# Optimization experiments

Hardware: AMD Instinct MI355X
Metric: run time of the kernel (lower is better)

## Reference

```python
import jax, jax.numpy as jnp
import numpy as np

N = 3072          # number of nodes
IN_DIM = 512
H = 8             # num_heads
D = 64            # out_dim per head
A = 8             # num_angles
CLAMP = 5.0


def setup_inputs() -> dict:
    key = jax.random.key(0)
    ks = jax.random.split(key, 9)
    HD = H * D
    return {
        "x": jax.random.normal(ks[0], (N, IN_DIM), jnp.float32),
        "node_rotation_angles": jax.random.normal(ks[1], (N, A), jnp.float32),
        "Wq": jax.random.normal(ks[2], (IN_DIM, HD), jnp.float32) * 0.05,
        "bq": jnp.zeros((HD,), jnp.float32),
        "Wk": jax.random.normal(ks[3], (IN_DIM, HD), jnp.float32) * 0.05,
        "bk": jnp.zeros((HD,), jnp.float32),
        "Wv": jax.random.normal(ks[4], (IN_DIM, HD), jnp.float32) * 0.05,
        "bv": jnp.zeros((HD,), jnp.float32),
        "S": jax.random.normal(ks[5], (A, HD // 2), jnp.float32),
    }


def reference(x, node_rotation_angles, Wq, bq, Wk, bk, Wv, bv, S):
    n = x.shape[0]
    # QKV projections -> [N, H, D]
    Qh = (x @ Wq + bq).reshape(n, H, D)
    Kh = (x @ Wk + bk).reshape(n, H, D)
    Vh = (x @ Wv + bv).reshape(n, H, D)

    # learned per-node rotation angles: [N, A] @ softmax(S, axis=1) -> [N, H*D/2]
    theta = node_rotation_angles @ jax.nn.softmax(S, axis=1)
    theta = jnp.repeat(theta, 2, axis=1).reshape(n, H, D)
    cos_pos = jnp.cos(theta)
    sin_pos = jnp.sin(theta)

    # torch.stack([-q_odd, q_even], dim=2).reshape -> concat of halves (faithful)
    q2 = jnp.concatenate([-Qh[..., 1::2], Qh[..., ::2]], axis=-1)
    k2 = jnp.concatenate([-Kh[..., 1::2], Kh[..., ::2]], axis=-1)
    Q = Qh * cos_pos + q2 * sin_pos
    K = Kh * cos_pos + k2 * sin_pos

    # faithful to original: raw .view() (reshape), NOT a transpose
    src = K.reshape(H, D, n)    # [H, D, N]
    dest = Q.reshape(H, n, D)   # [H, N, D]

    score = jnp.einsum("hnd,hdm->hnm", dest, src) / (D ** 0.5)
    score = jnp.clip(score, -CLAMP, CLAMP)
    attn = jax.nn.softmax(score, axis=-1)  # [H, N, N]

    # V uses a true transpose in the original
    msg = jnp.einsum("hnm,hmd->hnd", attn, jnp.swapaxes(Vh, 0, 1))
    return jnp.swapaxes(msg, 0, 1)  # [N, H, D]
```

## Files before the change

### kernel.cpp

```cpp
#include <hip/hip_runtime.h>

#define NN     3072
#define IND    512
#define NH     8
#define DH     64
#define HDTOT  512
#define NA     8
#define THALF  256
#define DN     196608

typedef float f32x4 __attribute__((ext_vector_type(4)));
typedef short bf16x8 __attribute__((ext_vector_type(8)));
typedef unsigned int u32x2 __attribute__((ext_vector_type(2)));

__device__ __forceinline__ unsigned short f2bf(float f) {
    union { float f; unsigned u; } a; a.f = f;
    unsigned u = a.u;
    return (unsigned short)((u + 0x7FFFu + ((u >> 16) & 1u)) >> 16);
}
__device__ __forceinline__ unsigned pack2(float a, float b) {
    union { float f; unsigned u; } ua, ub; ua.f = a; ub.f = b;
    unsigned ra = ua.u + 0x7FFFu + ((ua.u >> 16) & 1u);
    unsigned rb = ub.u + 0x7FFFu + ((ub.u >> 16) & 1u);
    return __builtin_amdgcn_perm(rb, ra, 0x07060302);
}
__device__ __forceinline__ float ubits2f(unsigned u) {
    union { unsigned u; float f; } c; c.u = u; return c.f;
}

__global__ __launch_bounds__(256) void k_prep(
    const float* __restrict__ S, const float* __restrict__ x,
    const float* __restrict__ Wq, const float* __restrict__ Wk,
    const float* __restrict__ Wv,
    float* __restrict__ SM, unsigned short* __restrict__ xb,
    unsigned short* __restrict__ WTb)
{
    __shared__ float sh[32 * 33];
    const int b = blockIdx.x, t = threadIdx.x;
    if (b == 0) {
        for (int a = 0; a < NA; ++a) {
            float v = S[a * THALF + t];
            sh[t] = v; __syncthreads();
            for (int s = 128; s > 0; s >>= 1) {
                if (t < s) sh[t] = fmaxf(sh[t], sh[t + s]);
                __syncthreads();
            }
            float mx = sh[0]; __syncthreads();
            float e = __expf(v - mx);
            sh[t] = e; __syncthreads();
            for (int s = 128; s > 0; s >>= 1) {
                if (t < s) sh[t] += sh[t + s];
                __syncthreads();
            }
            float inv = 1.0f / sh[0]; __syncthreads();
            SM[a * THALF + t] = e * inv;
        }
    } else if (b <= 768) {
        const size_t base = ((size_t)(b - 1) * 256 + t) * 8;
        float4 v0 = *reinterpret_cast<const float4*>(&x[base]);
        float4 v1 = *reinterpret_cast<const float4*>(&x[base + 4]);
        uint4 w;
        w.x = pack2(v0.x, v0.y); w.y = pack2(v0.z, v0.w);
        w.z = pack2(v1.x, v1.y); w.w = pack2(v1.z, v1.w);
        *reinterpret_cast<uint4*>(&xb[base]) = w;
    } else {
        const int b2 = b - 769;
        const int kt = b2 & 15, nt = b2 >> 4;
        const int k0 = kt * 32, n0 = nt * 32;
        const float* __restrict__ W = (n0 < 512) ? Wq : (n0 < 1024 ? Wk : Wv);
        const int nc0 = n0 & 511;
        const int r = t >> 5, c = t & 31;
        #pragma unroll
        for (int i = 0; i < 4; ++i)
            sh[(r + i * 8) * 33 + c] = W[(size_t)(k0 + r + i * 8) * HDTOT + nc0 + c];
        __syncthreads();
        #pragma unroll
        for (int i = 0; i < 4; ++i) {
            const int nr = r + i * 8;
            WTb[(size_t)(n0 + nr) * IND + k0 + c] = f2bf(sh[c * 33 + nr]);
        }
    }
}

__global__ __launch_bounds__(256) void k_qkv_mfma(
    const unsigned short* __restrict__ xb,
    const unsigned short* __restrict__ WTb,
    const float* __restrict__ bq, const float* __restrict__ bk,
    const float* __restrict__ bv,
    const float* __restrict__ angles, const float* __restrict__ SM,
    unsigned short* __restrict__ Qb, unsigned short* __restrict__ KTb,
    unsigned short* __restrict__ VTb)
{
    __shared__ __align__(16) char lds[41472];
    char* At  = lds;
    char* Bt  = lds + 16384;
    float* Cs = (float*)lds;
    float* SMl = (float*)(lds + 33280);

    const int t = threadIdx.x;
    const int lane = t & 63;
    const int wv = t >> 6;
    const int wrow = wv >> 1, wcol = wv & 1;
    const int l15 = lane & 15, lg = lane >> 4;
    const int r8 = lane >> 3, c8 = lane & 7;

    const int m0 = blockIdx.x * 128;
    const int n0 = blockIdx.y * 64;
    const int mat = n0 >> 9;
    const int c0 = n0 & 511;

    if (mat < 2) {
        #pragma unroll
        for (int r = 0; r < 8; ++r) SMl[r * 256 + t] = SM[r * 256 + t];
    }

    f32x4 acc[4][2];
    #pragma unroll
    for (int mf = 0; mf < 4; ++mf)
        #pragma unroll
        for (int nf = 0; nf < 2; ++nf)
            acc[mf][nf] = (f32x4){0.f, 0.f, 0.f, 0.f};

    for (int kt = 0; kt < 8; ++kt) {
        __syncthreads();
        #pragma unroll
        for (int i = 0; i < 4; ++i) {
            const int row = wv * 32 + i * 8 + r8;
            const unsigned short* src =
                xb + (size_t)(m0 + row) * IND + kt * 64 + (c8 ^ (row & 7)) * 8;
            __builtin_amdgcn_global_load_lds(
                (const __attribute__((address_space(1))) unsigned int*)src,
                (__attribute__((address_space(3))) unsigned int*)(At + (wv * 32 + i * 8) * 128),
                16, 0, 0);
        }
        #pragma unroll
        for (int i = 0; i < 2; ++i) {
            const int row = wv * 16 + i * 8 + r8;
            const unsigned short* src =
                WTb + (size_t)(n0 + row) * IND + kt * 64 + (c8 ^ (row & 7)) * 8;
            __builtin_amdgcn_global_load_lds(
                (const __attribute__((address_space(1))) unsigned int*)src,
                (__attribute__((address_space(3))) unsigned int*)(Bt + (wv * 16 + i * 8) * 128),
                16, 0, 0);
        }
        __syncthreads();
        #pragma unroll
        for (int ks = 0; ks < 2; ++ks) {
            bf16x8 af[4], bfr[2];
            #pragma unroll
            for (int mf = 0; mf < 4; ++mf) {
                const int row = wrow * 64 + mf * 16 + l15;
                int off = row * 128 + ks * 64 + lg * 16;
                off ^= (row & 7) << 4;
                af[mf] = *reinterpret_cast<const bf16x8*>(At + off);
            }
            #pragma unroll
            for (int nf = 0; nf < 2; ++nf) {
                const int row = wcol * 32 + nf * 16 + l15;
                int off = row * 128 + ks * 64 + lg * 16;
                off ^= (row & 7) << 4;
                bfr[nf] = *reinterpret_cast<const bf16x8*>(Bt + off);
            }
            #pragma unroll
            for (int mf = 0; mf < 4; ++mf)
                #pragma unroll
                for (int nf = 0; nf < 2; ++nf)
                    acc[mf][nf] = __builtin_amdgcn_mfma_f32_16x16x32_bf16(
                        af[mf], bfr[nf], acc[mf][nf], 0, 0, 0);
        }
    }

    if (mat == 2) {
        #pragma unroll
        for (int nf = 0; nf < 2; ++nf) {
            const int cg = c0 + wcol * 32 + nf * 16 + l15;
            const float b = bv[cg];
            const int hV = cg >> 6, dd = cg & 63;
            #pragma unroll
            for (int mf = 0; mf < 4; ++mf) {
                const int nb = m0 + wrow * 64 + mf * 16 + lg * 4;
                u32x2 w;
                w.x = pack2(acc[mf][nf][0] + b, acc[mf][nf][1] + b);
                w.y = pack2(acc[mf][nf][2] + b, acc[mf][nf][3] + b);
                *reinterpret_cast<u32x2*>(&VTb[(size_t)hV * DN + (size_t)dd * NN + nb]) = w;
            }
        }
        return;
    }

    __syncthreads();
    const float* __restrict__ bsv = mat ? bk : bq;
    #pragma unroll
    for (int nf = 0; nf < 2; ++nf) {
        const int colc = wcol * 32 + nf * 16 + l15;
        const float b = bsv[c0 + colc];
        #pragma unroll
        for (int mf = 0; mf < 4; ++mf) {
            const int rb = wrow * 64 + mf * 16 + lg * 4;
            #pragma unroll
            for (int r = 0; r < 4; ++r)
                Cs[(rb + r) * 65 + colc] = acc[mf][nf][r] + b;
        }
    }
    __syncthreads();

    const int ni0 = (t & 15) * 4;
    const int rbase = (t >> 4) * 8;
    const int pidx = (c0 + ni0) >> 1;
    const int hK = m0 / 384;
    const float QS = 0.1803368801111204f;

    #pragma unroll
    for (int rr = 0; rr < 8; ++rr) {
        const int row = rbase + rr;
        const int n = m0 + row;
        const float4 a0 = *reinterpret_cast<const float4*>(&angles[n * NA]);
        const float4 a1 = *reinterpret_cast<const float4*>(&angles[n * NA + 4]);
        float th0, th1;
        th0 = a0.x * SMl[0 * 256 + pidx];
        th0 = fmaf(a0.y, SMl[1 * 256 + pidx], th0);
        th0 = fmaf(a0.z, SMl[2 * 256 + pidx], th0);
        th0 = fmaf(a0.w, SMl[3 * 256 + pidx], th0);
        th0 = fmaf(a1.x, SMl[4 * 256 + pidx], th0);
        th0 = fmaf(a1.y, SMl[5 * 256 + pidx], th0);
        th0 = fmaf(a1.z, SMl[6 * 256 + pidx], th0);
        th0 = fmaf(a1.w, SMl[7 * 256 + pidx], th0);
        th1 = a0.x * SMl[0 * 256 + pidx + 1];
        th1 = fmaf(a0.y, SMl[1 * 256 + pidx + 1], th1);
        th1 = fmaf(a0.z, SMl[2 * 256 + pidx + 1], th1);
        th1 = fmaf(a0.w, SMl[3 * 256 + pidx + 1], th1);
        th1 = fmaf(a1.x, SMl[4 * 256 + pidx + 1], th1);
        th1 = fmaf(a1.y, SMl[5 * 256 + pidx + 1], th1);
        th1 = fmaf(a1.z, SMl[6 * 256 + pidx + 1], th1);
        th1 = fmaf(a1.w, SMl[7 * 256 + pidx + 1], th1);
        float s0, c0f, s1, c1f;
        __sincosf(th0, &s0, &c0f);
        __sincosf(th1, &s1, &c1f);
        float o[4];
        #pragma unroll
        for (int cc = 0; cc < 4; ++cc) {
            const int d = ni0 + cc;
            const int pd = (d < 32) ? (2 * d + 1) : (2 * (d - 32));
            float own = Cs[row * 65 + d];
            float pv  = Cs[row * 65 + pd];
            float q2  = (d < 32) ? -pv : pv;
            float ct  = (cc < 2) ? c0f : c1f;
            float st  = (cc < 2) ? s0 : s1;
            o[cc] = own * ct + q2 * st;
        }
        if (mat == 0) {
            u32x2 w;
            w.x = pack2(o[0] * QS, o[1] * QS);
            w.y = pack2(o[2] * QS, o[3] * QS);
            *reinterpret_cast<u32x2*>(&Qb[(size_t)n * HDTOT + c0 + ni0]) = w;
        } else {
            const int nn = n - hK * 384;
            const int dk = nn / 6;
            const int jb = (nn - dk * 6) * 512 + c0 + ni0;
            #pragma unroll
            for (int cc = 0; cc < 4; ++cc)
                KTb[(size_t)hK * DN + (size_t)(jb + cc) * 64 + dk] = f2bf(o[cc]);
        }
    }
}

template<int TILES, bool PARTIAL>
__global__ __launch_bounds__(128) void k_attn(
    const unsigned short* __restrict__ Qb,
    const unsigned short* __restrict__ KTb,
    const unsigned short* __restrict__ VTb,
    float* __restrict__ outp, float* __restrict__ Dp)
{
    __shared__ __align__(16) char smem[24576];
    const int t = threadIdx.x;
    const int lane = t & 63;
    const int wv = t >> 6;
    char* ktl = smem;
    char* vtl = smem + 8192;
    char* ptw = smem + 16384 + wv * 4096;

    const int h = blockIdx.y;
    const int qbase = blockIdx.x * 64;
    const int z = blockIdx.z;
    const int jt0 = z * TILES;
    const int l15 = lane & 15;
    const int lg = lane >> 4;
    const int r8 = lane >> 3;
    const int c8 = lane & 7;

    const float CLP = 7.2134752044448170f;

    const int X  = (l15 & 7) << 4;
    const int A0 = l15 * 128 + ((lg * 16) ^ X);
    const int A1 = l15 * 128 + ((64 + lg * 16) ^ X);
    const int W0 = l15 * 128 + ((lg * 8) ^ X);
    const int W1 = l15 * 128 + ((32 + lg * 8) ^ X);
    const int W2 = l15 * 128 + ((64 + lg * 8) ^ X);
    const int W3 = l15 * 128 + ((96 + lg * 8) ^ X);

    bf16x8 qf[2][2];
    #pragma unroll
    for (int im = 0; im < 2; ++im)
        #pragma unroll
        for (int ks = 0; ks < 2; ++ks) {
            const int i = qbase + wv * 32 + im * 16 + l15;
            qf[im][ks] = *reinterpret_cast<const bf16x8*>(
                Qb + (size_t)h * DN + (size_t)i * 64 + ks * 32 + lg * 8);
        }

    f32x4 oacc[2][4];
    #pragma unroll
    for (int im = 0; im < 2; ++im)
        #pragma unroll
        for (int db = 0; db < 4; ++db)
            oacc[im][db] = (f32x4){0.f, 0.f, 0.f, 0.f};
    float dpart[2] = {0.f, 0.f};

    for (int jj = 0; jj < TILES; ++jj) {
        const int j0 = (jt0 + jj) * 64;
        #pragma unroll
        for (int cc = 0; cc < 4; ++cc) {
            const int row = wv * 32 + cc * 8 + r8;
            const int chunk = c8 ^ (row & 7);
            const unsigned short* srcK =
                KTb + (size_t)h * DN + (size_t)(j0 + row) * 64 + chunk * 8;
            __builtin_amdgcn_global_load_lds(
                (const __attribute__((address_space(1))) unsigned int*)srcK,
                (__attribute__((address_space(3))) unsigned int*)(ktl + (wv * 32 + cc * 8) * 128),
                16, 0, 0);
            const unsigned short* srcV =
                VTb + (size_t)h * DN + (size_t)row * NN + j0 + chunk * 8;
            __builtin_amdgcn_global_load_lds(
                (const __attribute__((address_space(1))) unsigned int*)srcV,
                (__attribute__((address_space(3))) unsigned int*)(vtl + (wv * 32 + cc * 8) * 128),
                16, 0, 0);
        }
        __syncthreads();

        f32x4 sac[2][4];
        #pragma unroll
        for (int im = 0; im < 2; ++im)
            #pragma unroll
            for (int jb = 0; jb < 4; ++jb)
                sac[im][jb] = (f32x4){0.f, 0.f, 0.f, 0.f};
        #pragma unroll
        for (int ks = 0; ks < 2; ++ks) {
            const int Aks = ks ? A1 : A0;
            bf16x8 kf[4];
            #pragma unroll
            for (int jb = 0; jb < 4; ++jb)
                kf[jb] = *reinterpret_cast<const bf16x8*>(ktl + Aks + jb * 2048);
            #pragma unroll
            for (int im = 0; im < 2; ++im)
                #pragma unroll
                for (int jb = 0; jb < 4; ++jb)
                    sac[im][jb] = __builtin_amdgcn_mfma_f32_16x16x32_bf16(
                        kf[jb], qf[im][ks], sac[im][jb], 0, 0, 0);
        }

        #pragma unroll
        for (int im = 0; im < 2; ++im) {
            #pragma unroll
            for (int jb = 0; jb < 4; ++jb) {
                float p[4];
                #pragma unroll
                for (int r = 0; r < 4; ++r) {
                    float sc = __builtin_amdgcn_fmed3f(sac[im][jb][r], -CLP, CLP);
                    p[r] = __builtin_amdgcn_exp2f(sc);
                }
                dpart[im] += (p[0] + p[1]) + (p[2] + p[3]);
                u32x2 w;
                w.x = pack2(p[0], p[1]);
                w.y = pack2(p[2], p[3]);
                const int aw = (jb == 0) ? W0 : (jb == 1) ? W1 : (jb == 2) ? W2 : W3;
                *reinterpret_cast<u32x2*>(ptw + aw + im * 2048) = w;
            }
        }

        bf16x8 pf[2][2];
        #pragma unroll
        for (int im = 0; im < 2; ++im)
            #pragma unroll
            for (int js = 0; js < 2; ++js)
                pf[im][js] = *reinterpret_cast<const bf16x8*>(
                    ptw + (js ? A1 : A0) + im * 2048);
        #pragma unroll
        for (int js = 0; js < 2; ++js) {
            const int Ajs = js ? A1 : A0;
            #pragma unroll
            for (int db = 0; db < 4; ++db) {
                bf16x8 vf = *reinterpret_cast<const bf16x8*>(vtl + Ajs + db * 2048);
                #pragma unroll
                for (int im = 0; im < 2; ++im)
                    oacc[im][db] = __builtin_amdgcn_mfma_f32_16x16x32_bf16(
                        vf, pf[im][js], oacc[im][db], 0, 0, 0);
            }
        }
        __syncthreads();
    }

    #pragma unroll
    for (int im = 0; im < 2; ++im) {
        float d = dpart[im];
        d += __shfl_xor(d, 16);
        d += __shfl_xor(d, 32);
        const int i = qbase + wv * 32 + im * 16 + l15;
        if (PARTIAL) {
            if (lg == 0) Dp[((size_t)z * NH + h) * NN + i] = d;
            unsigned short* Ob = (unsigned short*)outp;
            const size_t base = (((size_t)z * NH + h) * NN + i) * 64;
            #pragma unroll
            for (int db = 0; db < 4; ++db) {
                u32x2 w;
                w.x = pack2(oacc[im][db][0], oacc[im][db][1]);
                w.y = pack2(oacc[im][db][2], oacc[im][db][3]);
                *reinterpret_cast<u32x2*>(&Ob[base + db * 16 + lg * 4]) = w;
            }
        } else {
            const float inv = 1.0f / d;
            #pragma unroll
            for (int db = 0; db < 4; ++db) {
                float4 o;
                o.x = oacc[im][db][0] * inv; o.y = oacc[im][db][1] * inv;
                o.z = oacc[im][db][2] * inv; o.w = oacc[im][db][3] * inv;
                *reinterpret_cast<float4*>(
                    &outp[(size_t)i * HDTOT + h * DH + db * 16 + lg * 4]) = o;
            }
        }
    }
}

__global__ __launch_bounds__(256) void k_reduce(
    const unsigned short* __restrict__ Ob, const float* __restrict__ Dp,
    float* __restrict__ out, int NZ)
{
    const int b  = blockIdx.x;
    const int t  = threadIdx.x;
    const int lo  = b & 7;
    const int mid = (b >> 3) % 6;
    const int hi  = b / 48;
    const int xq  = lo + 8 * mid;
    const int q   = hi * 256 + t;
    const int i   = xq * 64 + (q >> 7);
    const int h   = (q >> 4) & 7;
    const int dc  = q & 15;

    float o0 = 0.f, o1 = 0.f, o2 = 0.f, o3 = 0.f;
    float D = 0.f;
    for (int zz = 0; zz < NZ; ++zz) {
        u32x2 v = *reinterpret_cast<const u32x2*>(
            &Ob[(((size_t)zz * NH + h) * NN + i) * 64 + dc * 4]);
        o0 += ubits2f(v.x << 16);
        o1 += ubits2f(v.x & 0xFFFF0000u);
        o2 += ubits2f(v.y << 16);
        o3 += ubits2f(v.y & 0xFFFF0000u);
        D += Dp[((size_t)zz * NH + h) * NN + i];
    }
    const float inv = 1.0f / D;
    float4 w;
    w.x = o0 * inv; w.y = o1 * inv; w.z = o2 * inv; w.w = o3 * inv;
    *reinterpret_cast<float4*>(&out[(size_t)i * HDTOT + h * 64 + dc * 4]) = w;
}

extern "C" void kernel_launch(void* const* d_in, const int* in_sizes, int n_in,
                              void* d_out, int out_size, void* d_ws, size_t ws_size,
                              hipStream_t stream)
{
    const float* x      = (const float*)d_in[0];
    const float* angles = (const float*)d_in[1];
    const float* Wq     = (const float*)d_in[2];
    const float* bq     = (const float*)d_in[3];
    const float* Wk     = (const float*)d_in[4];
    const float* bk     = (const float*)d_in[5];
    const float* Wv     = (const float*)d_in[6];
    const float* bv     = (const float*)d_in[7];
    const float* S      = (const float*)d_in[8];
    float* out = (float*)d_out;

    float* ws = (float*)d_ws;
    float* SM = ws;
    unsigned short* xb  = (unsigned short*)(ws + 4096);
    unsigned short* WTb = xb + (size_t)NN * IND;
    unsigned short* Qb  = WTb + (size_t)1536 * IND;
    unsigned short* KTb = Qb + (size_t)NN * HDTOT;
    unsigned short* VTb = KTb + (size_t)NN * HDTOT;
    unsigned short* Opart = VTb + (size_t)NN * HDTOT;
    float* Dpart = (float*)(Opart + (size_t)4 * NH * NN * DH);
    const size_t need4 = (size_t)((char*)(Dpart + (size_t)4 * NH * NN) - (char*)d_ws);

    k_prep<<<1537, 256, 0, stream>>>(S, x, Wq, Wk, Wv, SM, xb, WTb);
    k_qkv_mfma<<<dim3(24, 24), 256, 0, stream>>>(xb, WTb, bq, bk, bv,
                                                 angles, SM, Qb, KTb, VTb);
    if (ws_size >= need4) {
        k_attn<12, true><<<dim3(48, 8, 4), 128, 0, stream>>>(Qb, KTb, VTb,
                                                             (float*)Opart, Dpart);
        k_reduce<<<1536, 256, 0, stream>>>(Opart, Dpart, out, 4);
    } else {
        k_attn<48, false><<<dim3(48, 8, 1), 128, 0, stream>>>(Qb, KTb, VTb, out, nullptr);
    }
}
```

Baseline: 75.30 us.

## Use 4-wave attention blocks over 128 queries, split keys six ways, shuffle softmax

Result: faster. 69.30 us (-8.0%).

```diff
diff --git a/kernel.cpp b/kernel.cpp
--- a/kernel.cpp
+++ b/kernel.cpp
@@ -8,6 +8,7 @@
 #define NA     8
 #define THALF  256
 #define DN     196608
+#define NZ     6
 
 typedef float f32x4 __attribute__((ext_vector_type(4)));
 typedef short bf16x8 __attribute__((ext_vector_type(8)));
@@ -38,22 +39,21 @@
     __shared__ float sh[32 * 33];
     const int b = blockIdx.x, t = threadIdx.x;
     if (b == 0) {
-        for (int a = 0; a < NA; ++a) {
-            float v = S[a * THALF + t];
-            sh[t] = v; __syncthreads();
-            for (int s = 128; s > 0; s >>= 1) {
-                if (t < s) sh[t] = fmaxf(sh[t], sh[t + s]);
-                __syncthreads();
-            }
-            float mx = sh[0]; __syncthreads();
-            float e = __expf(v - mx);
-            sh[t] = e; __syncthreads();
-            for (int s = 128; s > 0; s >>= 1) {
-                if (t < s) sh[t] += sh[t + s];
-                __syncthreads();
-            }
-            float inv = 1.0f / sh[0]; __syncthreads();
-            SM[a * THALF + t] = e * inv;
+        const int wvp = t >> 6;
+        const int ln  = t & 63;
+        for (int a = wvp; a < NA; a += 4) {
+            float4 v = *reinterpret_cast<const float4*>(&S[a * THALF + ln * 4]);
+            float mx = fmaxf(fmaxf(v.x, v.y), fmaxf(v.z, v.w));
+            #pragma unroll
+            for (int m = 1; m < 64; m <<= 1) mx = fmaxf(mx, __shfl_xor(mx, m));
+            float e0 = __expf(v.x - mx), e1 = __expf(v.y - mx);
+            float e2 = __expf(v.z - mx), e3 = __expf(v.w - mx);
+            float s = (e0 + e1) + (e2 + e3);
+            #pragma unroll
+            for (int m = 1; m < 64; m <<= 1) s += __shfl_xor(s, m);
+            float inv = 1.0f / s;
+            float4 o; o.x = e0 * inv; o.y = e1 * inv; o.z = e2 * inv; o.w = e3 * inv;
+            *reinterpret_cast<float4*>(&SM[a * THALF + ln * 4]) = o;
         }
     } else if (b <= 768) {
         const size_t base = ((size_t)(b - 1) * 256 + t) * 8;
@@ -265,13 +265,13 @@
 }
 
 template<int TILES, bool PARTIAL>
-__global__ __launch_bounds__(128) void k_attn(
+__global__ __launch_bounds__(256) void k_attn(
     const unsigned short* __restrict__ Qb,
     const unsigned short* __restrict__ KTb,
     const unsigned short* __restrict__ VTb,
     float* __restrict__ outp, float* __restrict__ Dp)
 {
-    __shared__ __align__(16) char smem[24576];
+    __shared__ __align__(16) char smem[32768];
     const int t = threadIdx.x;
     const int lane = t & 63;
     const int wv = t >> 6;
@@ -280,7 +280,7 @@
     char* ptw = smem + 16384 + wv * 4096;
 
     const int h = blockIdx.y;
-    const int qbase = blockIdx.x * 64;
+    const int qbase = blockIdx.x * 128;
     const int z = blockIdx.z;
     const int jt0 = z * TILES;
     const int l15 = lane & 15;
@@ -319,20 +319,20 @@
     for (int jj = 0; jj < TILES; ++jj) {
         const int j0 = (jt0 + jj) * 64;
         #pragma unroll
-        for (int cc = 0; cc < 4; ++cc) {
-            const int row = wv * 32 + cc * 8 + r8;
+        for (int cc = 0; cc < 2; ++cc) {
+            const int row = wv * 16 + cc * 8 + r8;
             const int chunk = c8 ^ (row & 7);
             const unsigned short* srcK =
                 KTb + (size_t)h * DN + (size_t)(j0 + row) * 64 + chunk * 8;
             __builtin_amdgcn_global_load_lds(
                 (const __attribute__((address_space(1))) unsigned int*)srcK,
-                (__attribute__((address_space(3))) unsigned int*)(ktl + (wv * 32 + cc * 8) * 128),
+                (__attribute__((address_space(3))) unsigned int*)(ktl + (wv * 16 + cc * 8) * 128),
                 16, 0, 0);
             const unsigned short* srcV =
                 VTb + (size_t)h * DN + (size_t)row * NN + j0 + chunk * 8;
             __builtin_amdgcn_global_load_lds(
                 (const __attribute__((address_space(1))) unsigned int*)srcV,
-                (__attribute__((address_space(3))) unsigned int*)(vtl + (wv * 32 + cc * 8) * 128),
+                (__attribute__((address_space(3))) unsigned int*)(vtl + (wv * 16 + cc * 8) * 128),
                 16, 0, 0);
         }
         __syncthreads();
@@ -432,7 +432,7 @@
 
 __global__ __launch_bounds__(256) void k_reduce(
     const unsigned short* __restrict__ Ob, const float* __restrict__ Dp,
-    float* __restrict__ out, int NZ)
+    float* __restrict__ out, int nz)
 {
     const int b  = blockIdx.x;
     const int t  = threadIdx.x;
@@ -447,7 +447,7 @@
 
     float o0 = 0.f, o1 = 0.f, o2 = 0.f, o3 = 0.f;
     float D = 0.f;
-    for (int zz = 0; zz < NZ; ++zz) {
+    for (int zz = 0; zz < nz; ++zz) {
         u32x2 v = *reinterpret_cast<const u32x2*>(
             &Ob[(((size_t)zz * NH + h) * NN + i) * 64 + dc * 4]);
         o0 += ubits2f(v.x << 16);
@@ -485,17 +485,17 @@
     unsigned short* KTb = Qb + (size_t)NN * HDTOT;
     unsigned short* VTb = KTb + (size_t)NN * HDTOT;
     unsigned short* Opart = VTb + (size_t)NN * HDTOT;
-    float* Dpart = (float*)(Opart + (size_t)4 * NH * NN * DH);
-    const size_t need4 = (size_t)((char*)(Dpart + (size_t)4 * NH * NN) - (char*)d_ws);
+    float* Dpart = (float*)(Opart + (size_t)NZ * NH * NN * DH);
+    const size_t need = (size_t)((char*)(Dpart + (size_t)NZ * NH * NN) - (char*)d_ws);
 
     k_prep<<<1537, 256, 0, stream>>>(S, x, Wq, Wk, Wv, SM, xb, WTb);
     k_qkv_mfma<<<dim3(24, 24), 256, 0, stream>>>(xb, WTb, bq, bk, bv,
                                                  angles, SM, Qb, KTb, VTb);
-    if (ws_size >= need4) {
-        k_attn<12, true><<<dim3(48, 8, 4), 128, 0, stream>>>(Qb, KTb, VTb,
-                                                             (float*)Opart, Dpart);
-        k_reduce<<<1536, 256, 0, stream>>>(Opart, Dpart, out, 4);
+    if (ws_size >= need) {
+        k_attn<48 / NZ, true><<<dim3(24, 8, NZ), 256, 0, stream>>>(Qb, KTb, VTb,
+                                                                   (float*)Opart, Dpart);
+        k_reduce<<<1536, 256, 0, stream>>>(Opart, Dpart, out, NZ);
     } else {
-        k_attn<48, false><<<dim3(48, 8, 1), 128, 0, stream>>>(Qb, KTb, VTb, out, nullptr);
-    }
-}
+        k_attn<48, false><<<dim3(24, 8, 1), 256, 0, stream>>>(Qb, KTb, VTb, out, nullptr);
+    }
+}
```
